# Performance work log

Measured on AMD Instinct MI355X. Metric: run time of the kernel, lower is better.

## Reference

```python
import jax, jax.numpy as jnp
import numpy as np

B, C, H, W, E, HEADS = 8, 128, 96, 96, 16, 4
HD = C // HEADS

def _ln(x, g, b, eps=1e-5):
    m = jnp.mean(x, axis=-1, keepdims=True)
    v = jnp.mean(jnp.square(x - m), axis=-1, keepdims=True)
    return (x - m) * jax.lax.rsqrt(v + eps) * g + b

def _gelu(x):
    return jax.nn.gelu(x, approximate=False)  # torch nn.GELU default (erf)

def setup_inputs() -> dict:
    key = jax.random.key(0)
    ks = iter(jax.random.split(key, 48))
    def wgt(shape, s=0.02):
        return jax.random.normal(next(ks), shape, jnp.float32) * s
    d = {
        "feature_map": jax.random.normal(next(ks), (B, C, H, W), jnp.float32),
        "hyperedge_scores": jax.random.uniform(next(ks), (B, H * W, E), jnp.float32),
        # norm_node_pre
        "np_g": jnp.ones((C,), jnp.float32), "np_b": jnp.zeros((C,), jnp.float32),
        # MultiheadAttention (self-attn over hyperedges)
        "mha_w_in": wgt((3 * C, C)), "mha_b_in": jnp.zeros((3 * C,), jnp.float32),
        "mha_w_out": wgt((C, C)), "mha_b_out": jnp.zeros((C,), jnp.float32),
        # transformer FFN
        "ffn_w1": wgt((2 * C, C)), "ffn_b1": jnp.zeros((2 * C,), jnp.float32),
        "ffn_w2": wgt((C, 2 * C)), "ffn_b2": jnp.zeros((C,), jnp.float32),
        # shared LayerNorm inside HypergraphTransformerConv (used twice)
        "tnorm_g": jnp.ones((C,), jnp.float32), "tnorm_b": jnp.zeros((C,), jnp.float32),
        # norm_hyper
        "nh_g": jnp.ones((C,), jnp.float32), "nh_b": jnp.zeros((C,), jnp.float32),
        # hyper_proj
        "hp_w": wgt((C, C)), "hp_b": jnp.zeros((C,), jnp.float32),
        # HyperedgeGuidedNodeAttention
        "q_w": wgt((C, C)), "q_b": jnp.zeros((C,), jnp.float32),
        "kv_w": wgt((2 * C, C)), "kv_b": jnp.zeros((2 * C,), jnp.float32),
        # norm_fusion
        "nf_g": jnp.ones((2 * C,), jnp.float32), "nf_b": jnp.zeros((2 * C,), jnp.float32),
        # gate = Linear(2C->C) + LayerNorm(C) + Sigmoid
        "gate_w": wgt((C, 2 * C)), "gate_b": jnp.zeros((C,), jnp.float32),
        "gate_ln_g": jnp.ones((C,), jnp.float32), "gate_ln_b": jnp.zeros((C,), jnp.float32),
        # node_proj
        "nproj_w": wgt((C, C)), "nproj_b": jnp.zeros((C,), jnp.float32),
    }
    return d

def _forward(feature_map, hyperedge_scores, np_g, np_b, mha_w_in, mha_b_in,
             mha_w_out, mha_b_out, ffn_w1, ffn_b1, ffn_w2, ffn_b2,
             tnorm_g, tnorm_b, nh_g, nh_b, hp_w, hp_b, q_w, q_b, kv_w, kv_b,
             nf_g, nf_b, gate_w, gate_b, gate_ln_g, gate_ln_b, nproj_w, nproj_b):
    b, c, h, w = feature_map.shape
    n = h * w
    node = jnp.transpose(feature_map.reshape(b, c, n), (0, 2, 1))   # [B,N,C]
    node = _ln(node, np_g, np_b)
    # hyperedge aggregation: H^T @ X -> [B,E,C]
    hyper = jnp.einsum('bne,bnc->bec', hyperedge_scores, node)
    # --- HypergraphTransformerConv (self-attn over E=16 hyperedges) ---
    qkv = hyper @ mha_w_in.T + mha_b_in                               # [B,E,3C]
    q, k, v = jnp.split(qkv, 3, axis=-1)
    def heads(x):  # [B,E,C] -> [B,h,E,hd]
        return jnp.transpose(x.reshape(b, E, HEADS, HD), (0, 2, 1, 3))
    q, k, v = heads(q), heads(k), heads(v)
    attn = jax.nn.softmax(jnp.einsum('bhqd,bhkd->bhqk', q, k) / np.sqrt(HD), axis=-1)
    ao = jnp.einsum('bhqk,bhkd->bhqd', attn, v)
    ao = jnp.transpose(ao, (0, 2, 1, 3)).reshape(b, E, c)
    ao = ao @ mha_w_out.T + mha_b_out
    x = _ln(hyper + ao, tnorm_g, tnorm_b)
    ffn = _gelu(x @ ffn_w1.T + ffn_b1) @ ffn_w2.T + ffn_b2
    hyper = _ln(x + ffn, tnorm_g, tnorm_b)
    # ---
    hyper = _ln(hyper, nh_g, nh_b)
    hyper = _gelu(hyper @ hp_w.T + hp_b)                              # [B,E,C]
    intra = jnp.einsum('bne,bec->bnc', hyperedge_scores, hyper)       # [B,N,C]
    # HyperedgeGuidedNodeAttention (scale = C**-0.5)
    Q = node @ q_w.T + q_b
    K, V = jnp.split(hyper @ kv_w.T + kv_b, 2, axis=-1)
    a = jax.nn.softmax(jnp.einsum('bnc,bec->bne', Q, K) * (c ** -0.5), axis=-1)
    cross = jnp.einsum('bne,bec->bnc', a, V)
    combined = _ln(jnp.concatenate([intra, cross], axis=-1), nf_g, nf_b)
    gate = jax.nn.sigmoid(_ln(combined @ gate_w.T + gate_b, gate_ln_g, gate_ln_b))
    fused = gate * intra + (1.0 - gate) * cross
    upd = node + fused                                                # dropout in eval mode
    out = _gelu(upd @ nproj_w.T + nproj_b)
    return jnp.transpose(out, (0, 2, 1)).reshape(b, c, h, w)

def reference(feature_map, hyperedge_scores, np_g, np_b, mha_w_in, mha_b_in,
              mha_w_out, mha_b_out, ffn_w1, ffn_b1, ffn_w2, ffn_b2,
              tnorm_g, tnorm_b, nh_g, nh_b, hp_w, hp_b, q_w, q_b, kv_w, kv_b,
              nf_g, nf_b, gate_w, gate_b, gate_ln_g, gate_ln_b, nproj_w, nproj_b):
    return _forward(feature_map, hyperedge_scores, np_g, np_b, mha_w_in, mha_b_in,
                    mha_w_out, mha_b_out, ffn_w1, ffn_b1, ffn_w2, ffn_b2,
                    tnorm_g, tnorm_b, nh_g, nh_b, hp_w, hp_b, q_w, q_b, kv_w, kv_b,
                    nf_g, nf_b, gate_w, gate_b, gate_ln_g, gate_ln_b, nproj_w, nproj_b)
```

## Files before the change

kernel.cpp:

```cpp
#include <hip/hip_runtime.h>

typedef unsigned short bf_t;
typedef unsigned int u32;
typedef short short8 __attribute__((ext_vector_type(8)));
typedef float f32x4 __attribute__((ext_vector_type(4)));

#define NB 8
#define CC 128
#define NN 9216
#define EE 16
#define NT 144
#define HS 24

__device__ __forceinline__ float b2f(bf_t u){ return __uint_as_float(((u32)u)<<16); }
__device__ __forceinline__ bf_t f2b(float f){
  u32 u = __float_as_uint(f);
  u = (u + 0x7fffu + ((u>>16)&1u)) >> 16;
  return (bf_t)u;
}
__device__ __forceinline__ float gelu_f(float x){ return 0.5f*x*(1.f+erff(x*0.70710678118654752f)); }
__device__ __forceinline__ float red16(float v){
  #pragma unroll
  for (int m=1;m<16;m<<=1) v += __shfl_xor(v, m, 16);
  return v;
}
__device__ __forceinline__ float grs(float var){
  return rsqrtf(fmaxf(var + 1e-5f, 1e-8f));
}
__device__ __forceinline__ short8 ldw8(const float* __restrict__ p){
  float4 a = *(const float4*)p;
  float4 b = *(const float4*)(p+4);
  short8 o;
  o[0]=(short)f2b(a.x); o[1]=(short)f2b(a.y); o[2]=(short)f2b(a.z); o[3]=(short)f2b(a.w);
  o[4]=(short)f2b(b.x); o[5]=(short)f2b(b.y); o[6]=(short)f2b(b.z); o[7]=(short)f2b(b.w);
  return o;
}

template<int MODE>
__global__ __launch_bounds__(256) void k_pre(float* __restrict__ hacc,
    const float* __restrict__ gw, const float* __restrict__ npw,
    bf_t* __restrict__ gwb, bf_t* __restrict__ npwb,
    const float* __restrict__ w_in, const float* __restrict__ w_out,
    const float* __restrict__ w1, const float* __restrict__ w2,
    const float* __restrict__ hpw, const float* __restrict__ kvw,
    const float* __restrict__ qw,
    bf_t* __restrict__ w_in_b, bf_t* __restrict__ w_out_b,
    bf_t* __restrict__ w1_b, bf_t* __restrict__ w2_b,
    bf_t* __restrict__ hpw_b, bf_t* __restrict__ kvw_b,
    bf_t* __restrict__ qwT_b){
  int i = blockIdx.x*256 + threadIdx.x;
  hacc[i] = 0.f;
  if (MODE >= 1){
    gwb[i]       = f2b(gw[i]);
    gwb[i+16384] = f2b(gw[i+16384]);
    npwb[i]      = f2b(npw[i]);
  }
  if (MODE == 2){
    #pragma unroll
    for (int k=0;k<3;k++) w_in_b[i + k*16384] = f2b(w_in[i + k*16384]);
    w_out_b[i]       = f2b(w_out[i]);
    w1_b[i]          = f2b(w1[i]);
    w1_b[i+16384]    = f2b(w1[i+16384]);
    w2_b[i]          = f2b(w2[i]);
    w2_b[i+16384]    = f2b(w2[i+16384]);
    hpw_b[i]         = f2b(hpw[i]);
    kvw_b[i]         = f2b(kvw[i]);
    kvw_b[i+16384]   = f2b(kvw[i+16384]);
    qwT_b[i]         = f2b(qw[(i&127)*128 + (i>>7)]);
  }
}

template<int BFOUT, int AGG>
__global__ __launch_bounds__(256,4) void k_ln_agg(const float* __restrict__ fm,
                                                  const float* __restrict__ g,
                                                  const float* __restrict__ bb,
                                                  const float* __restrict__ sc,
                                                  float* __restrict__ nln,
                                                  bf_t* __restrict__ nlnb,
                                                  float* __restrict__ hacc){
  int b = blockIdx.y, n0 = blockIdx.x*64, tid = threadIdx.x;
  __shared__ float xs[128*65];
  __shared__ float scs[64][17];
  __shared__ float ps[4][64], pq[4][64], mrs[2][64];
  const float* base = fm + (size_t)b*CC*NN + n0;
  #pragma unroll
  for (int p=0;p<8;p++){
    int idx = tid + p*256;
    int c = idx>>4, n4 = (idx&15)*4;
    float4 v = *(const float4*)(base + (size_t)c*NN + n4);
    xs[c*65 + n4+0] = v.x; xs[c*65 + n4+1] = v.y;
    xs[c*65 + n4+2] = v.z; xs[c*65 + n4+3] = v.w;
  }
  if (AGG){
    int n = tid>>2, e4 = (tid&3)*4;
    float4 sv = *(const float4*)(sc + ((size_t)(b*NN + n0 + n))*EE + e4);
    scs[n][e4+0] = sv.x; scs[n][e4+1] = sv.y;
    scs[n][e4+2] = sv.z; scs[n][e4+3] = sv.w;
  }
  __syncthreads();
  { int cg = tid>>6, n = tid&63;
    float s=0.f, q=0.f;
    #pragma unroll
    for (int c=0;c<32;c++){ float v = xs[(cg*32+c)*65 + n]; s+=v; q+=v*v; }
    ps[cg][n]=s; pq[cg][n]=q;
  }
  __syncthreads();
  if (tid < 64){
    float S = ps[0][tid]+ps[1][tid]+ps[2][tid]+ps[3][tid];
    float Q = pq[0][tid]+pq[1][tid]+pq[2][tid]+pq[3][tid];
    float m = S*(1.f/128.f);
    mrs[0][tid] = m; mrs[1][tid] = grs(Q*(1.f/128.f) - m*m);
  }
  __syncthreads();
  #pragma unroll
  for (int p=0;p<8;p++){
    int idx = tid + p*256;
    int c = idx>>4, n4 = (idx&15)*4;
    float gv = g[c], bv = bb[c];
    float v0 = (xs[c*65+n4+0]-mrs[0][n4+0])*mrs[1][n4+0]*gv + bv;
    float v1 = (xs[c*65+n4+1]-mrs[0][n4+1])*mrs[1][n4+1]*gv + bv;
    float v2 = (xs[c*65+n4+2]-mrs[0][n4+2])*mrs[1][n4+2]*gv + bv;
    float v3 = (xs[c*65+n4+3]-mrs[0][n4+3])*mrs[1][n4+3]*gv + bv;
    xs[c*65+n4+0]=v0; xs[c*65+n4+1]=v1; xs[c*65+n4+2]=v2; xs[c*65+n4+3]=v3;
    if (!BFOUT){
      float4 o; o.x=v0; o.y=v1; o.z=v2; o.w=v3;
      *(float4*)(nln + ((size_t)(b*CC + c))*NN + n0 + n4) = o;
    }
  }
  __syncthreads();
  if (BFOUT){
    #pragma unroll
    for (int p=0;p<4;p++){
      int idx = tid + p*256;
      int n = idx>>4, c8 = (idx&15)*8;
      short8 o;
      #pragma unroll
      for (int j=0;j<8;j++) o[j] = (short)f2b(xs[(c8+j)*65 + n]);
      *(short8*)(nlnb + ((size_t)(b*NN + n0 + n))*CC + c8) = o;
    }
  }
  if (AGG){
    int cp = tid&63, eh = tid>>6;
    float a0[4]={0,0,0,0}, a1[4]={0,0,0,0};
    for (int n=0;n<64;n++){
      float x0 = xs[cp*65 + n], x1 = xs[(cp+64)*65 + n];
      #pragma unroll
      for (int j=0;j<4;j++){
        float se = scs[n][eh*4+j];
        a0[j] += se*x0; a1[j] += se*x1;
      }
    }
    #pragma unroll
    for (int j=0;j<4;j++){
      float* hb = hacc + (size_t)(b*EE + eh*4 + j)*CC;
      atomicAdd(hb + cp, a0[j]);
      atomicAdd(hb + cp + 64, a1[j]);
    }
  }
}

template<int K, int NOUT, int ACT, int WB, int NW>
__device__ __forceinline__ void gemm16(const bf_t* A, int SA,
                                       const float* __restrict__ W,
                                       const bf_t* __restrict__ Wb,
                                       const float* __restrict__ bias,
                                       bf_t* O, int SO, int tid){
  int lane = tid&63, wid = tid>>6;
  int m16 = lane&15, quad = lane>>4;
  for (int t0 = wid; t0 < NOUT/16; t0 += NW){
    int n0 = t0*16;
    f32x4 acc = {0.f,0.f,0.f,0.f};
    #pragma unroll
    for (int k0=0;k0<K;k0+=32){
      short8 af = *(const short8*)(A + m16*SA + k0 + quad*8);
      short8 bfv = WB ? *(const short8*)(Wb + (size_t)(n0+m16)*K + k0 + quad*8)
                      : ldw8(W + (size_t)(n0+m16)*K + k0 + quad*8);
      acc = __builtin_amdgcn_mfma_f32_16x16x32_bf16(af, bfv, acc, 0, 0, 0);
    }
    int col = n0 + m16;
    float bv = bias[col];
    #pragma unroll
    for (int r=0;r<4;r++){
      float v = acc[r] + bv;
      if (ACT) v = gelu_f(v);
      O[(quad*4+r)*SO + col] = f2b(v);
    }
  }
}

#define SP1 136
#define SP2 264
#define SP3 392

template<int WB>
__global__ __launch_bounds__(512) void k_edge(const float* __restrict__ hacc,
    const float* w_in, const float* b_in, const float* w_out, const float* b_out,
    const float* w1, const float* b1, const float* w2, const float* b2v,
    const float* tg, const float* tb, const float* nhg, const float* nhb,
    const float* hpw, const float* hpb, const float* kvw, const float* kvbias,
    const float* qw, const float* qb,
    const bf_t* __restrict__ w_in_b, const bf_t* __restrict__ w_out_b,
    const bf_t* __restrict__ w1_b, const bf_t* __restrict__ w2_b,
    const bf_t* __restrict__ hpw_b, const bf_t* __restrict__ kvw_b,
    const bf_t* __restrict__ qwT_b,
    bf_t* __restrict__ hfw, bf_t* __restrict__ vws,
    bf_t* __restrict__ Ktgb, float* __restrict__ qbK){
  __shared__ __align__(16) bf_t hyp0[16*SP1];
  __shared__ __align__(16) bf_t qkvb[16*SP3];
  __shared__ __align__(16) bf_t aob [16*SP1];
  __shared__ __align__(16) bf_t xnb [16*SP1];
  __shared__ __align__(16) bf_t h1b [16*SP2];
  __shared__ __align__(16) bf_t t2b [16*SP1];
  __shared__ __align__(16) bf_t hfb [16*SP1];
  __shared__ __align__(16) bf_t kvo [16*SP2];
  int b = blockIdx.x, tid = threadIdx.x;
  int lane = tid&63, wid = tid>>6, m16 = lane&15, quad = lane>>4;

  #pragma unroll
  for (int p=0;p<4;p++){
    int idx = tid + p*512;
    int e = idx>>7, c = idx&127;
    hyp0[e*SP1 + c] = f2b(hacc[(size_t)(b*EE + e)*CC + c]);
  }
  __syncthreads();
  gemm16<128,384,0,WB,8>(hyp0, SP1, w_in, w_in_b, b_in, qkvb, SP3, tid);
  __syncthreads();
  if (tid < 256){
    int part = tid&3, hq = tid>>2;
    int h = hq>>4, qi = hq&15;
    int dbase = h*32 + part*8;
    float qv[8];
    #pragma unroll
    for (int j=0;j<8;j++) qv[j] = b2f(qkvb[qi*SP3 + dbase + j]);
    float dot[16];
    #pragma unroll
    for (int kk=0;kk<16;kk++){
      float s = 0.f;
      #pragma unroll
      for (int j=0;j<8;j++) s += qv[j]*b2f(qkvb[kk*SP3 + 128 + dbase + j]);
      dot[kk] = s;
    }
    #pragma unroll
    for (int m=1;m<4;m<<=1){
      #pragma unroll
      for (int kk=0;kk<16;kk++) dot[kk] += __shfl_xor(dot[kk], m, 4);
    }
    const float sc1 = 0.17677669529663687f;
    float mx = -1e30f;
    #pragma unroll
    for (int kk=0;kk<16;kk++){ dot[kk] *= sc1; mx = fmaxf(mx, dot[kk]); }
    float sum = 0.f;
    #pragma unroll
    for (int kk=0;kk<16;kk++){ dot[kk] = __expf(dot[kk]-mx); sum += dot[kk]; }
    float inv = 1.f/sum;
    float ao[8] = {0,0,0,0,0,0,0,0};
    #pragma unroll
    for (int kk=0;kk<16;kk++){
      float p = dot[kk]*inv;
      #pragma unroll
      for (int j=0;j<8;j++) ao[j] += p*b2f(qkvb[kk*SP3 + 256 + dbase + j]);
    }
    #pragma unroll
    for (int j=0;j<8;j++) aob[qi*SP1 + dbase + j] = f2b(ao[j]);
  }
  __syncthreads();
  gemm16<128,128,0,WB,8>(aob, SP1, w_out, w_out_b, b_out, xnb, SP1, tid);
  __syncthreads();
  if (tid < 256){
    int e = tid>>4, i = tid&15;
    float v[8]; float s=0.f, q=0.f;
    #pragma unroll
    for (int j=0;j<8;j++){
      int c = i*8+j;
      v[j] = b2f(hyp0[e*SP1+c]) + b2f(xnb[e*SP1+c]);
      s += v[j]; q += v[j]*v[j];
    }
    s = red16(s); q = red16(q);
    float m = s*(1.f/128.f);
    float rs = grs(q*(1.f/128.f) - m*m);
    #pragma unroll
    for (int j=0;j<8;j++){
      int c = i*8+j;
      xnb[e*SP1+c] = f2b((v[j]-m)*rs*tg[c] + tb[c]);
    }
  }
  __syncthreads();
  gemm16<128,256,1,WB,8>(xnb, SP1, w1, w1_b, b1, h1b, SP2, tid);
  __syncthreads();
  gemm16<256,128,0,WB,8>(h1b, SP2, w2, w2_b, b2v, aob, SP1, tid);
  __syncthreads();
  if (tid < 256){
    int e = tid>>4, i = tid&15;
    float v[8]; float s=0.f, q=0.f;
    #pragma unroll
    for (int j=0;j<8;j++){
      int c = i*8+j;
      v[j] = b2f(xnb[e*SP1+c]) + b2f(aob[e*SP1+c]);
      s += v[j]; q += v[j]*v[j];
    }
    s = red16(s); q = red16(q);
    float m = s*(1.f/128.f);
    float rs = grs(q*(1.f/128.f) - m*m);
    float s2=0.f, q2=0.f;
    #pragma unroll
    for (int j=0;j<8;j++){
      int c = i*8+j;
      v[j] = (v[j]-m)*rs*tg[c] + tb[c];
      s2 += v[j]; q2 += v[j]*v[j];
    }
    s2 = red16(s2); q2 = red16(q2);
    float m2 = s2*(1.f/128.f);
    float rs2 = grs(q2*(1.f/128.f) - m2*m2);
    #pragma unroll
    for (int j=0;j<8;j++){
      int c = i*8+j;
      t2b[e*SP1+c] = f2b((v[j]-m2)*rs2*nhg[c] + nhb[c]);
    }
  }
  __syncthreads();
  gemm16<128,128,1,WB,8>(t2b, SP1, hpw, hpw_b, hpb, hfb, SP1, tid);
  __syncthreads();
  gemm16<128,256,0,WB,8>(hfb, SP1, kvw, kvw_b, kvbias, kvo, SP2, tid);
  __syncthreads();
  #pragma unroll
  for (int p=0;p<4;p++){
    int idx = tid + p*512;
    int e = idx>>7, c = idx&127;
    size_t o = (size_t)(b*EE + e)*CC + c;
    hfw[o] = hfb[e*SP1 + c];
    vws[o] = kvo[e*SP2 + 128 + c];
  }
  {
    int n0 = wid*16;
    f32x4 acc = {0.f,0.f,0.f,0.f};
    #pragma unroll
    for (int k0=0;k0<128;k0+=32){
      short8 a = *(const short8*)(kvo + m16*SP2 + k0 + quad*8);
      short8 bq;
      if (WB){
        bq = *(const short8*)(qwT_b + (size_t)(n0+m16)*128 + k0 + quad*8);
      } else {
        #pragma unroll
        for (int j=0;j<8;j++)
          bq[j] = (short)f2b(qw[(size_t)(k0+quad*8+j)*128 + n0+m16]);
      }
      acc = __builtin_amdgcn_mfma_f32_16x16x32_bf16(a, bq, acc, 0, 0, 0);
    }
    #pragma unroll
    for (int r=0;r<4;r++)
      Ktgb[(size_t)(b*EE + quad*4 + r)*CC + n0 + m16] = f2b(acc[r]);
  }
  if (tid < 256){
    int e = tid>>4, i = tid&15;
    float s = 0.f;
    #pragma unroll
    for (int j=0;j<8;j++) s += qb[i*8+j]*b2f(kvo[e*SP2 + i*8+j]);
    s = red16(s);
    if (i == 0) qbK[b*EE + e] = s;
  }
}

template<int MODE>
__global__ __launch_bounds__(256,3) void k_meganode(
    float* __restrict__ io, const bf_t* __restrict__ nlnb,
    const float* __restrict__ sc,
    const bf_t* __restrict__ hf, const bf_t* __restrict__ vw,
    const bf_t* __restrict__ ktg, const float* __restrict__ qbK,
    const float* __restrict__ nfg, const float* __restrict__ nfb,
    const float* __restrict__ gw, const bf_t* __restrict__ gwb,
    const float* __restrict__ gb,
    const float* __restrict__ glng, const float* __restrict__ glnb,
    const float* __restrict__ npw, const bf_t* __restrict__ npwb,
    const float* __restrict__ npb){
  int tid = threadIdx.x, lane = tid&63, wid = tid>>6;
  int m16 = lane&15, quad = lane>>4;
  int b = blockIdx.y, n0 = blockIdx.x*64;
  __shared__ __align__(16) char sm[46336];
  bf_t* xt  = (bf_t*)(sm);
  bf_t* ktT = (bf_t*)(sm + 17408);
  bf_t* hfT = (bf_t*)(sm + 21760);
  bf_t* vfT = (bf_t*)(sm + 27904);
  bf_t* ash = (bf_t*)(sm + 34048);
  bf_t* ct  = (bf_t*)(sm + 37120);
  const short8 z8 = {0,0,0,0,0,0,0,0};

  if (MODE == 2){
    const bf_t* nb = nlnb + ((size_t)(b*NN + n0))*CC;
    #pragma unroll
    for (int p=0;p<4;p++){
      int idx = tid + p*256;
      int n = idx>>4, c8 = (idx&15)*8;
      *(short8*)&xt[n*136 + c8] = *(const short8*)(nb + (size_t)n*CC + c8);
    }
  } else {
    #pragma unroll
    for (int p=0;p<8;p++){
      int idx = tid + p*256;
      int c = idx>>4, n4 = (idx&15)*4;
      float4 v = *(const float4*)(io + ((size_t)(b*CC + c))*NN + n0 + n4);
      xt[(n4+0)*136 + c] = f2b(v.x);
      xt[(n4+1)*136 + c] = f2b(v.y);
      xt[(n4+2)*136 + c] = f2b(v.z);
      xt[(n4+3)*136 + c] = f2b(v.w);
    }
  }
  { const u32* kp = (const u32*)(ktg + (size_t)b*EE*CC);
    #pragma unroll
    for (int p=0;p<4;p++){
      int idx = tid + p*256;
      int e = idx>>6, c2 = (idx&63)*2;
      *(u32*)&ktT[e*136 + c2] = kp[idx];
    }
  }
  { const u32* hs = (const u32*)(hf + (size_t)b*EE*CC);
    const u32* vs = (const u32*)(vw + (size_t)b*EE*CC);
    #pragma unroll
    for (int p=0;p<4;p++){
      int idx = tid + p*256;
      int e = idx>>6, c2 = (idx&63)*2;
      u32 hv = hs[idx], vv = vs[idx];
      hfT[(c2+0)*HS + e] = (bf_t)(hv&0xffffu);
      hfT[(c2+1)*HS + e] = (bf_t)(hv>>16);
      vfT[(c2+0)*HS + e] = (bf_t)(vv&0xffffu);
      vfT[(c2+1)*HS + e] = (bf_t)(vv>>16);
    }
  }
  __syncthreads();

  f32x4 dacc = {0.f,0.f,0.f,0.f};
  #pragma unroll
  for (int kk=0;kk<4;kk++){
    short8 a = *(const short8*)(xt + (wid*16+m16)*136 + kk*32 + quad*8);
    short8 bfr = *(const short8*)(ktT + m16*136 + kk*32 + quad*8);
    dacc = __builtin_amdgcn_mfma_f32_16x16x32_bf16(a, bfr, dacc, 0, 0, 0);
  }
  { float qbe = qbK[b*EE + m16];
    #pragma unroll
    for (int r=0;r<4;r++){
      float v = (dacc[r] + qbe) * 0.08838834764831845f;
      float m = v;
      #pragma unroll
      for (int msk=1;msk<16;msk<<=1) m = fmaxf(m, __shfl_xor(m, msk, 16));
      float ex = __expf(v - m);
      float s = ex;
      #pragma unroll
      for (int msk=1;msk<16;msk<<=1) s += __shfl_xor(s, msk, 16);
      ash[(wid*16 + quad*4 + r)*HS + m16] = f2b(ex / s);
    }
  }

  short8 scf = z8, asf = z8;
  if (quad < 2){
    const float* sp = sc + ((size_t)(b*NN + n0 + wid*16 + m16))*EE + quad*8;
    float4 u0 = *(const float4*)sp;
    float4 u1 = *(const float4*)(sp+4);
    scf[0]=(short)f2b(u0.x); scf[1]=(short)f2b(u0.y); scf[2]=(short)f2b(u0.z); scf[3]=(short)f2b(u0.w);
    scf[4]=(short)f2b(u1.x); scf[5]=(short)f2b(u1.y); scf[6]=(short)f2b(u1.z); scf[7]=(short)f2b(u1.w);
    asf = *(const short8*)(ash + (wid*16+m16)*HS + quad*8);
  }
  f32x4 acc_it[8], acc_cr[8];
  #pragma unroll
  for (int t=0;t<8;t++){
    short8 bh = z8, bv = z8;
    if (quad < 2){
      bh = *(const short8*)(hfT + (t*16+m16)*HS + quad*8);
      bv = *(const short8*)(vfT + (t*16+m16)*HS + quad*8);
    }
    f32x4 zf = {0.f,0.f,0.f,0.f};
    acc_it[t] = __builtin_amdgcn_mfma_f32_16x16x32_bf16(scf, bh, zf, 0, 0, 0);
    acc_cr[t] = __builtin_amdgcn_mfma_f32_16x16x32_bf16(asf, bv, zf, 0, 0, 0);
  }

  float mean4[4], rstd4[4];
  { float s4[4]={0,0,0,0}, q4[4]={0,0,0,0};
    #pragma unroll
    for (int t=0;t<8;t++)
      #pragma unroll
      for (int r=0;r<4;r++){
        float a = acc_it[t][r], c = acc_cr[t][r];
        s4[r] += a + c; q4[r] += a*a + c*c;
      }
    #pragma unroll
    for (int r=0;r<4;r++){
      s4[r] = red16(s4[r]); q4[r] = red16(q4[r]);
      mean4[r] = s4[r]*(1.f/256.f);
      rstd4[r] = grs(q4[r]*(1.f/256.f) - mean4[r]*mean4[r]);
    }
  }
  __syncthreads();
  short8 af[8];
  #pragma unroll
  for (int s=0;s<2;s++){
    #pragma unroll
    for (int r=0;r<4;r++){
      int node = wid*16 + quad*4 + r;
      #pragma unroll
      for (int t=0;t<4;t++){
        int ch = (s*4+t)*16 + m16;
        ct[node*72 + t*16 + m16] = f2b((acc_it[s*4+t][r]-mean4[r])*rstd4[r]*nfg[ch] + nfb[ch]);
      }
    }
    #pragma unroll
    for (int k2=0;k2<2;k2++)
      af[s*2+k2] = *(const short8*)(ct + (wid*16+m16)*72 + k2*32 + quad*8);
  }
  #pragma unroll
  for (int s=0;s<2;s++){
    #pragma unroll
    for (int r=0;r<4;r++){
      int node = wid*16 + quad*4 + r;
      #pragma unroll
      for (int t=0;t<4;t++){
        int ch = (s*4+t)*16 + m16;
        ct[node*72 + t*16 + m16] = f2b((acc_cr[s*4+t][r]-mean4[r])*rstd4[r]*nfg[128+ch] + nfb[128+ch]);
      }
    }
    #pragma unroll
    for (int k2=0;k2<2;k2++)
      af[4+s*2+k2] = *(const short8*)(ct + (wid*16+m16)*72 + k2*32 + quad*8);
  }

  f32x4 acc_g[8];
  #pragma unroll
  for (int t=0;t<8;t++){
    f32x4 a = {0.f,0.f,0.f,0.f};
    #pragma unroll
    for (int kk=0;kk<8;kk++){
      short8 w8 = (MODE >= 1) ? *(const short8*)(gwb + (size_t)(t*16+m16)*256 + kk*32 + quad*8)
                              : ldw8(gw + (size_t)(t*16+m16)*256 + kk*32 + quad*8);
      a = __builtin_amdgcn_mfma_f32_16x16x32_bf16(af[kk], w8, a, 0, 0, 0);
    }
    acc_g[t] = a;
  }

  float m2r[4], rs2r[4];
  { float s2[4]={0,0,0,0}, q2[4]={0,0,0,0};
    #pragma unroll
    for (int t=0;t<8;t++){
      float bv = gb[t*16+m16];
      #pragma unroll
      for (int r=0;r<4;r++){
        float v = acc_g[t][r] + bv;
        acc_g[t][r] = v; s2[r] += v; q2[r] += v*v;
      }
    }
    #pragma unroll
    for (int r=0;r<4;r++){
      s2[r] = red16(s2[r]); q2[r] = red16(q2[r]);
      m2r[r] = s2[r]*(1.f/128.f);
      rs2r[r] = grs(q2[r]*(1.f/128.f) - m2r[r]*m2r[r]);
    }
  }

  #pragma unroll
  for (int t=0;t<8;t++){
    short8 bh = z8, bv = z8;
    if (quad < 2){
      bh = *(const short8*)(hfT + (t*16+m16)*HS + quad*8);
      bv = *(const short8*)(vfT + (t*16+m16)*HS + quad*8);
    }
    f32x4 zf = {0.f,0.f,0.f,0.f};
    f32x4 itR = __builtin_amdgcn_mfma_f32_16x16x32_bf16(scf, bh, zf, 0, 0, 0);
    f32x4 crR = __builtin_amdgcn_mfma_f32_16x16x32_bf16(asf, bv, zf, 0, 0, 0);
    int col = t*16 + m16;
    float lg = glng[col], lb = glnb[col];
    #pragma unroll
    for (int r=0;r<4;r++){
      float z = (acc_g[t][r]-m2r[r])*rs2r[r]*lg + lb;
      float gs = 1.f/(1.f + __expf(-z));
      int node = wid*16 + quad*4 + r;
      float nld = b2f(xt[node*136 + col]);
      xt[node*136 + col] = f2b(nld + gs*itR[r] + (1.f-gs)*crR[r]);
    }
  }

  short8 bfu[4];
  #pragma unroll
  for (int kk=0;kk<4;kk++)
    bfu[kk] = *(const short8*)(xt + (wid*16+m16)*136 + kk*32 + quad*8);
  #pragma unroll
  for (int mt=0;mt<8;mt++){
    f32x4 o = {0.f,0.f,0.f,0.f};
    #pragma unroll
    for (int kk=0;kk<4;kk++){
      short8 aw = (MODE >= 1) ? *(const short8*)(npwb + (size_t)(mt*16+m16)*128 + kk*32 + quad*8)
                              : ldw8(npw + (size_t)(mt*16+m16)*128 + kk*32 + quad*8);
      o = __builtin_amdgcn_mfma_f32_16x16x32_bf16(aw, bfu[kk], o, 0, 0, 0);
    }
    #pragma unroll
    for (int r=0;r<4;r++){
      int cp = mt*16 + quad*4 + r;
      io[((size_t)(b*CC + cp))*NN + n0 + wid*16 + m16] = gelu_f(o[r] + npb[cp]);
    }
  }
}

extern "C" void kernel_launch(void* const* d_in, const int* in_sizes, int n_in,
                              void* d_out, int out_size, void* d_ws, size_t ws_size,
                              hipStream_t stream){
  (void)in_sizes; (void)n_in; (void)out_size;
  const float* fm   = (const float*)d_in[0];
  const float* sc   = (const float*)d_in[1];
  const float* npg  = (const float*)d_in[2];
  const float* npb_ = (const float*)d_in[3];
  const float* w_in = (const float*)d_in[4];
  const float* b_in = (const float*)d_in[5];
  const float* w_out= (const float*)d_in[6];
  const float* b_out= (const float*)d_in[7];
  const float* w1   = (const float*)d_in[8];
  const float* b1   = (const float*)d_in[9];
  const float* w2   = (const float*)d_in[10];
  const float* b2v  = (const float*)d_in[11];
  const float* tg   = (const float*)d_in[12];
  const float* tb   = (const float*)d_in[13];
  const float* nhg  = (const float*)d_in[14];
  const float* nhb  = (const float*)d_in[15];
  const float* hpw  = (const float*)d_in[16];
  const float* hpb  = (const float*)d_in[17];
  const float* qw   = (const float*)d_in[18];
  const float* qb   = (const float*)d_in[19];
  const float* kvw  = (const float*)d_in[20];
  const float* kvb  = (const float*)d_in[21];
  const float* nfg  = (const float*)d_in[22];
  const float* nfb  = (const float*)d_in[23];
  const float* gw   = (const float*)d_in[24];
  const float* gb   = (const float*)d_in[25];
  const float* glng = (const float*)d_in[26];
  const float* glnb = (const float*)d_in[27];
  const float* npw  = (const float*)d_in[28];
  const float* npb2 = (const float*)d_in[29];

  float* nln = (float*)d_out;

  char* w = (char*)d_ws;
  float* hacc    = (float*)(w);
  float* qbK     = (float*)(w + 65536);
  bf_t*  hfw     = (bf_t*) (w + 66048);
  bf_t*  vws     = (bf_t*) (w + 98816);
  bf_t*  Ktgb    = (bf_t*) (w + 131584);
  bf_t*  gwb     = (bf_t*) (w + 164352);
  bf_t*  npwb    = (bf_t*) (w + 229888);
  bf_t*  w_in_b  = (bf_t*) (w + 262656);
  bf_t*  w_out_b = (bf_t*) (w + 360960);
  bf_t*  w1_b    = (bf_t*) (w + 393728);
  bf_t*  w2_b    = (bf_t*) (w + 459264);
  bf_t*  hpw_b   = (bf_t*) (w + 524800);
  bf_t*  kvw_b   = (bf_t*) (w + 557568);
  bf_t*  qwT_b   = (bf_t*) (w + 623104);
  bf_t*  nlnb    = (bf_t*) (w + 655872);
  bool full  = (ws_size >= (size_t)19530240);
  bool pre   = (ws_size >= (size_t)262656);

  if (full){
    k_pre<2><<<dim3(64), dim3(256), 0, stream>>>(hacc, gw, npw, gwb, npwb,
        w_in, w_out, w1, w2, hpw, kvw, qw,
        w_in_b, w_out_b, w1_b, w2_b, hpw_b, kvw_b, qwT_b);
    k_ln_agg<1,1><<<dim3(NT,8), dim3(256), 0, stream>>>(fm, npg, npb_, sc, nln, nlnb, hacc);
    k_edge<1><<<dim3(8), dim3(512), 0, stream>>>(hacc, w_in,b_in,w_out,b_out,
        w1,b1,w2,b2v, tg,tb, nhg,nhb, hpw,hpb, kvw,kvb, qw,qb,
        w_in_b, w_out_b, w1_b, w2_b, hpw_b, kvw_b, qwT_b,
        hfw, vws, Ktgb, qbK);
    k_meganode<2><<<dim3(NT,8), dim3(256), 0, stream>>>(nln, nlnb, sc, hfw, vws, Ktgb, qbK,
        nfg, nfb, gw, gwb, gb, glng, glnb, npw, npwb, npb2);
  } else if (pre){
    k_pre<1><<<dim3(64), dim3(256), 0, stream>>>(hacc, gw, npw, gwb, npwb,
        w_in, w_out, w1, w2, hpw, kvw, qw,
        w_in_b, w_out_b, w1_b, w2_b, hpw_b, kvw_b, qwT_b);
    k_ln_agg<0,1><<<dim3(NT,8), dim3(256), 0, stream>>>(fm, npg, npb_, sc, nln, nlnb, hacc);
    k_edge<0><<<dim3(8), dim3(512), 0, stream>>>(hacc, w_in,b_in,w_out,b_out,
        w1,b1,w2,b2v, tg,tb, nhg,nhb, hpw,hpb, kvw,kvb, qw,qb,
        w_in_b, w_out_b, w1_b, w2_b, hpw_b, kvw_b, qwT_b,
        hfw, vws, Ktgb, qbK);
    k_meganode<1><<<dim3(NT,8), dim3(256), 0, stream>>>(nln, nlnb, sc, hfw, vws, Ktgb, qbK,
        nfg, nfb, gw, gwb, gb, glng, glnb, npw, npwb, npb2);
  } else {
    k_pre<0><<<dim3(64), dim3(256), 0, stream>>>(hacc, gw, npw, gwb, npwb,
        w_in, w_out, w1, w2, hpw, kvw, qw,
        w_in_b, w_out_b, w1_b, w2_b, hpw_b, kvw_b, qwT_b);
    k_ln_agg<0,1><<<dim3(NT,8), dim3(256), 0, stream>>>(fm, npg, npb_, sc, nln, nlnb, hacc);
    k_edge<0><<<dim3(8), dim3(512), 0, stream>>>(hacc, w_in,b_in,w_out,b_out,
        w1,b1,w2,b2v, tg,tb, nhg,nhb, hpw,hpb, kvw,kvb, qw,qb,
        w_in_b, w_out_b, w1_b, w2_b, hpw_b, kvw_b, qwT_b,
        hfw, vws, Ktgb, qbK);
    k_meganode<0><<<dim3(NT,8), dim3(256), 0, stream>>>(nln, nlnb, sc, hfw, vws, Ktgb, qbK,
        nfg, nfb, gw, gwb, gb, glng, glnb, npw, npwb, npb2);
  }
}
```

Baseline: 253.8 us.

## Recompute intra/cross MFMA products and alias LDS to raise occupancy to 4

The kernel no longer keeps 16 f32x4 accumulators for the intra and cross products live across the LayerNorm statistics pass. It recomputes the cheap K=16 MFMAs when writing normalized values to shared memory. LDS is also shrunk by aliasing the ct buffer onto the ktT region and reordering buffers, and launch bounds go from 3 to 4 blocks per SIMD. The intent is lower register and LDS pressure so more waves stay resident, at the cost of doing those MFMAs twice. The aliasing is only safe if ktT is dead before ct is written.

```diff
diff --git a/kernel.cpp b/kernel.cpp
--- a/kernel.cpp
+++ b/kernel.cpp
@@ -361,7 +361,7 @@
 }
 
 template<int MODE>
-__global__ __launch_bounds__(256,3) void k_meganode(
+__global__ __launch_bounds__(256,4) void k_meganode(
     float* __restrict__ io, const bf_t* __restrict__ nlnb,
     const float* __restrict__ sc,
     const bf_t* __restrict__ hf, const bf_t* __restrict__ vw,
@@ -375,13 +375,13 @@
   int tid = threadIdx.x, lane = tid&63, wid = tid>>6;
   int m16 = lane&15, quad = lane>>4;
   int b = blockIdx.y, n0 = blockIdx.x*64;
-  __shared__ __align__(16) char sm[46336];
+  __shared__ __align__(16) char sm[38912];
   bf_t* xt  = (bf_t*)(sm);
-  bf_t* ktT = (bf_t*)(sm + 17408);
-  bf_t* hfT = (bf_t*)(sm + 21760);
-  bf_t* vfT = (bf_t*)(sm + 27904);
+  bf_t* hfT = (bf_t*)(sm + 17408);
+  bf_t* vfT = (bf_t*)(sm + 23552);
+  bf_t* ktT = (bf_t*)(sm + 29696);
   bf_t* ash = (bf_t*)(sm + 34048);
-  bf_t* ct  = (bf_t*)(sm + 37120);
+  bf_t* ct  = (bf_t*)(sm + 29696);
   const short8 z8 = {0,0,0,0,0,0,0,0};
 
   if (MODE == 2){
@@ -458,28 +458,24 @@
     scf[4]=(short)f2b(u1.x); scf[5]=(short)f2b(u1.y); scf[6]=(short)f2b(u1.z); scf[7]=(short)f2b(u1.w);
     asf = *(const short8*)(ash + (wid*16+m16)*HS + quad*8);
   }
-  f32x4 acc_it[8], acc_cr[8];
-  #pragma unroll
-  for (int t=0;t<8;t++){
-    short8 bh = z8, bv = z8;
-    if (quad < 2){
-      bh = *(const short8*)(hfT + (t*16+m16)*HS + quad*8);
-      bv = *(const short8*)(vfT + (t*16+m16)*HS + quad*8);
-    }
-    f32x4 zf = {0.f,0.f,0.f,0.f};
-    acc_it[t] = __builtin_amdgcn_mfma_f32_16x16x32_bf16(scf, bh, zf, 0, 0, 0);
-    acc_cr[t] = __builtin_amdgcn_mfma_f32_16x16x32_bf16(asf, bv, zf, 0, 0, 0);
-  }
 
   float mean4[4], rstd4[4];
   { float s4[4]={0,0,0,0}, q4[4]={0,0,0,0};
     #pragma unroll
-    for (int t=0;t<8;t++)
+    for (int t=0;t<8;t++){
+      short8 bh = z8, bv = z8;
+      if (quad < 2){
+        bh = *(const short8*)(hfT + (t*16+m16)*HS + quad*8);
+        bv = *(const short8*)(vfT + (t*16+m16)*HS + quad*8);
+      }
+      f32x4 zf = {0.f,0.f,0.f,0.f};
+      f32x4 it = __builtin_amdgcn_mfma_f32_16x16x32_bf16(scf, bh, zf, 0, 0, 0);
+      f32x4 cr = __builtin_amdgcn_mfma_f32_16x16x32_bf16(asf, bv, zf, 0, 0, 0);
       #pragma unroll
       for (int r=0;r<4;r++){
-        float a = acc_it[t][r], c = acc_cr[t][r];
-        s4[r] += a + c; q4[r] += a*a + c*c;
+        s4[r] += it[r] + cr[r]; q4[r] += it[r]*it[r] + cr[r]*cr[r];
       }
+    }
     #pragma unroll
     for (int r=0;r<4;r++){
       s4[r] = red16(s4[r]); q4[r] = red16(q4[r]);
@@ -488,16 +484,22 @@
     }
   }
   __syncthreads();
+
   short8 af[8];
   #pragma unroll
   for (int s=0;s<2;s++){
     #pragma unroll
-    for (int r=0;r<4;r++){
-      int node = wid*16 + quad*4 + r;
-      #pragma unroll
-      for (int t=0;t<4;t++){
-        int ch = (s*4+t)*16 + m16;
-        ct[node*72 + t*16 + m16] = f2b((acc_it[s*4+t][r]-mean4[r])*rstd4[r]*nfg[ch] + nfb[ch]);
+    for (int tp=0;tp<4;tp++){
+      int t = s*4 + tp;
+      short8 bh = z8;
+      if (quad < 2) bh = *(const short8*)(hfT + (t*16+m16)*HS + quad*8);
+      f32x4 zf = {0.f,0.f,0.f,0.f};
+      f32x4 it = __builtin_amdgcn_mfma_f32_16x16x32_bf16(scf, bh, zf, 0, 0, 0);
+      #pragma unroll
+      for (int r=0;r<4;r++){
+        int node = wid*16 + quad*4 + r;
+        int ch = t*16 + m16;
+        ct[node*72 + tp*16 + m16] = f2b((it[r]-mean4[r])*rstd4[r]*nfg[ch] + nfb[ch]);
       }
     }
     #pragma unroll
@@ -507,12 +509,17 @@
   #pragma unroll
   for (int s=0;s<2;s++){
     #pragma unroll
-    for (int r=0;r<4;r++){
-      int node = wid*16 + quad*4 + r;
-      #pragma unroll
-      for (int t=0;t<4;t++){
-        int ch = (s*4+t)*16 + m16;
-        ct[node*72 + t*16 + m16] = f2b((acc_cr[s*4+t][r]-mean4[r])*rstd4[r]*nfg[128+ch] + nfb[128+ch]);
+    for (int tp=0;tp<4;tp++){
+      int t = s*4 + tp;
+      short8 bv = z8;
+      if (quad < 2) bv = *(const short8*)(vfT + (t*16+m16)*HS + quad*8);
+      f32x4 zf = {0.f,0.f,0.f,0.f};
+      f32x4 cr = __builtin_amdgcn_mfma_f32_16x16x32_bf16(asf, bv, zf, 0, 0, 0);
+      #pragma unroll
+      for (int r=0;r<4;r++){
+        int node = wid*16 + quad*4 + r;
+        int ch = t*16 + m16;
+        ct[node*72 + tp*16 + m16] = f2b((cr[r]-mean4[r])*rstd4[r]*nfg[128+ch] + nfb[128+ch]);
       }
     }
     #pragma unroll
```

Result: slower. 263.8 us (+3.9%).
